# Performance work log

Hardware: AMD Instinct MI355X
Metric: run time of the kernel (lower is better)

## Reference

```python
import jax, jax.numpy as jnp
import numpy as np

NUM_GRAPHS = 128
EPS = 1e-5  # torch BatchNorm1d default eps


def setup_inputs() -> dict:
    key = jax.random.key(0)
    ks = jax.random.split(key, 24)
    N, E, NHE = 50000, 800000, 50000
    NODE_RAW, HEDGE_RAW, H, HH, HOUT = 92, 40, 128, 128, 256
    s = 0.05
    inp = {
        "x": jax.random.normal(ks[0], (N, NODE_RAW), jnp.float32),
        "hedge_attrs": jax.random.normal(ks[1], (NHE, HEDGE_RAW), jnp.float32),
        "inter_relations_index": jax.random.randint(ks[2], (3, E), 0, N, jnp.int64),
        "batch": jax.random.randint(ks[3], (N,), 0, NUM_GRAPHS, jnp.int64),
        "num_nodes": N,
        # embed: Linear(92, h_dim)
        "embed_w": jax.random.normal(ks[4], (NODE_RAW, H), jnp.float32) * s,
        "embed_b": jax.random.normal(ks[5], (H,), jnp.float32) * s,
        # bembed: Linear(hedge_dim, hidden_hedge_dim)
        "bembed_w": jax.random.normal(ks[6], (HEDGE_RAW, HH), jnp.float32) * s,
        "bembed_b": jax.random.normal(ks[7], (HH,), jnp.float32) * s,
        # conv.lin_full_presplit: Linear(2H+HH, 2H)
        "lin_w": jax.random.normal(ks[8], (2 * H + HH, 2 * H), jnp.float32) * s,
        "lin_b": jax.random.normal(ks[9], (2 * H,), jnp.float32) * s,
        "bn1_g": jnp.ones((2 * H,), jnp.float32),
        "bn1_b": jnp.zeros((2 * H,), jnp.float32),
        "bn2_g": jnp.ones((H,), jnp.float32),
        "bn2_b": jnp.zeros((H,), jnp.float32),
        # learnable temperature of SoftmaxAggregation (init 1.0)
        "aggr_t": jnp.ones((), jnp.float32),
        "l1_w": jax.random.normal(ks[10], (H, HOUT), jnp.float32) * s,
        "l1_b": jax.random.normal(ks[11], (HOUT,), jnp.float32) * s,
        "out_w": jax.random.normal(ks[12], (HOUT, 1), jnp.float32) * s,
        "out_b": jax.random.normal(ks[13], (1,), jnp.float32) * s,
    }
    return inp


def _batchnorm(z, g, b):
    mu = z.mean(axis=0)
    var = z.var(axis=0)  # biased, matching torch training-mode normalization
    return (z - mu) * jax.lax.rsqrt(var + EPS) * g + b


def reference(x, hedge_attrs, inter_relations_index, batch, num_nodes,
              embed_w, embed_b, bembed_w, bembed_b, lin_w, lin_b,
              bn1_g, bn1_b, bn2_g, bn2_b, aggr_t, l1_w, l1_b, out_w, out_b):
    idx0 = inter_relations_index[0]
    idx1 = inter_relations_index[1]
    connect_feats = hedge_attrs @ bembed_w + bembed_b          # [NHE, HH]
    h = x @ embed_w + embed_b                                   # [N, H]

    # --- CHGInterConv ---
    origin = h[idx0]                                            # [E, H]
    connect = connect_feats[idx1]                               # [E, HH]
    remote = h[idx0]                                            # faithful to source (uses idx0)
    z = jnp.concatenate([origin, connect, remote], axis=1)      # [E, 2H+HH]
    z = z @ lin_w + lin_b                                       # [E, 2H]
    z = _batchnorm(z, bn1_g, bn1_b)
    z_f, z_c = jnp.split(z, 2, axis=-1)
    msg = jax.nn.sigmoid(z_f) * jax.nn.softplus(z_c)            # [E, H]

    # learned SoftmaxAggregation: per-node, per-channel segment softmax of t*msg
    alpha = msg * aggr_t
    m = jax.ops.segment_max(alpha, idx0, num_segments=num_nodes)
    m = jnp.where(jnp.isfinite(m), m, 0.0)                      # empty segments
    e = jnp.exp(alpha - m[idx0])
    denom = jax.ops.segment_sum(e, idx0, num_segments=num_nodes)
    w = e / (denom[idx0] + 1e-16)
    out = jax.ops.segment_sum(msg * w, idx0, num_segments=num_nodes)  # [N, H]

    out = _batchnorm(out, bn2_g, bn2_b)
    h = jax.nn.softplus(out + h)                                # residual + softplus

    # --- global mean pool over graphs ---
    counts = jax.ops.segment_sum(jnp.ones((num_nodes,), h.dtype), batch,
                                 num_segments=NUM_GRAPHS)
    pooled = jax.ops.segment_sum(h, batch, num_segments=NUM_GRAPHS)
    pooled = pooled / jnp.maximum(counts, 1.0)[:, None]         # [G, H]

    g = jax.nn.softplus(pooled @ l1_w + l1_b)                   # [G, HOUT]
    return g @ out_w + out_b                                    # [G, 1]
```

## Files before the change

kernel.cpp:

```cpp
#include <hip/hip_runtime.h>
#include <hip/hip_bf16.h>


#define EPS_BN 1e-5f
#define LOG2E 1.4426950408889634f
#define LN2   0.6931471805599453f

#define BIN_SH 8
#define BIN_CHUNK 4096

typedef __attribute__((ext_vector_type(8))) short bf16x8;
typedef __attribute__((ext_vector_type(4))) float f32x4;
typedef __attribute__((ext_vector_type(2))) float f32x2;

__device__ __forceinline__ float fexp2(float x) {
#if __has_builtin(__builtin_amdgcn_exp2f)
    return __builtin_amdgcn_exp2f(x);
#else
    return __expf(x * LN2);
#endif
}
__device__ __forceinline__ float flog2(float x) {
#if __has_builtin(__builtin_amdgcn_logf)
    return __builtin_amdgcn_logf(x);
#else
    return __logf(x) * LOG2E;
#endif
}
__device__ __forceinline__ float softplus_fast(float x) {
    return LN2 * flog2(1.f + fexp2(x * LOG2E));
}

__device__ __forceinline__ f32x2 pk_fma2(f32x2 a, f32x2 b, f32x2 c) {
#if __has_builtin(__builtin_elementwise_fma)
    return __builtin_elementwise_fma(a, b, c);
#else
    return (f32x2){fmaf(a.x, b.x, c.x), fmaf(a.y, b.y, c.y)};
#endif
}

__device__ __forceinline__ unsigned short f2bf(float f) {
    unsigned u = __float_as_uint(f);
    unsigned r = (u + 0x7fffu + ((u >> 16) & 1u)) >> 16;
    return (unsigned short)r;
}
__device__ __forceinline__ float bflo(unsigned u) { return __uint_as_float(u << 16); }
__device__ __forceinline__ float bfhi(unsigned u) { return __uint_as_float(u & 0xffff0000u); }
__device__ __forceinline__ float bfu16(unsigned short v) { return __uint_as_float(((unsigned)v) << 16); }
__device__ __forceinline__ unsigned pack2bf(float x, float y) {
    return (unsigned)f2bf(x) | ((unsigned)f2bf(y) << 16);
}

#if __has_builtin(__builtin_amdgcn_cvt_pk_f32_fp8) && __has_builtin(__builtin_amdgcn_cvt_pk_fp8_f32)
#define HW_FP8 1
#else
#define HW_FP8 0
#endif

__device__ __forceinline__ unsigned char f2fp8(float f) {
#if HW_FP8
    int r = __builtin_amdgcn_cvt_pk_fp8_f32(f, f, 0, false);
    return (unsigned char)(r & 0xff);
#else
    unsigned u = __float_as_uint(f);
    unsigned s = (u >> 24) & 0x80u;
    float af = fabsf(f);
    if (!(af >= 0.015625f)) {
        int m = (int)rintf(af * 512.f);
        if (m > 7) m = 7;
        return (unsigned char)(s | (unsigned)m);
    }
    if (af > 448.f) return (unsigned char)(s | 0x7e);
    unsigned au = __float_as_uint(af);
    unsigned r = au + 0x7ffffu + ((au >> 20) & 1u);
    int e8 = (int)(r >> 23) - 120;
    unsigned m = (r >> 20) & 7u;
    if (e8 > 15 || (e8 == 15 && m == 7)) return (unsigned char)(s | 0x7e);
    return (unsigned char)(s | ((unsigned)e8 << 3) | m);
#endif
}

__device__ __forceinline__ void fp8pair(unsigned p, f32x2& lo, f32x2& hi) {
#if HW_FP8
    lo = __builtin_amdgcn_cvt_pk_f32_fp8((int)p, false);
    hi = __builtin_amdgcn_cvt_pk_f32_fp8((int)p, true);
#else
    auto dec = [](unsigned byte) -> float {
        unsigned s = (byte & 0x80u) << 24;
        unsigned em = byte & 0x7fu;
        float nrm = __uint_as_float(s | ((em << 20) + 0x3C000000u));
        float sub = __uint_as_float(s | 0x3F800000u) * (float)em * 0.001953125f;
        return (em >= 8) ? nrm : sub;
    };
    lo = (f32x2){dec(p & 0xff), dec((p >> 8) & 0xff)};
    hi = (f32x2){dec((p >> 16) & 0xff), dec(p >> 24)};
#endif
}

__device__ __forceinline__ int perm256(int j) {
    return (j < 128) ? ((j >> 1) * 4 + (j & 1)) : (((j - 128) >> 1) * 4 + 2 + (j & 1));
}

__global__ __launch_bounds__(256) void k_pre(const float* __restrict__ ew, const float* __restrict__ bw,
                                             const float* __restrict__ lw,
                                             unsigned short* __restrict__ embB, unsigned short* __restrict__ bembB,
                                             unsigned short* __restrict__ waB, unsigned short* __restrict__ wcB,
                                             const int* __restrict__ idx0, const int* __restrict__ batch,
                                             int* __restrict__ bsum, int* __restrict__ gcount,
                                             int E, int N, int NB) {
    const int t = threadIdx.x;
    const int bid = blockIdx.x;
    if (bid >= 320) {
        __shared__ int lhist[256];
        __shared__ int lbat[128];
        const int cb = bid - 320;
        lhist[t] = 0;
        if (t < 128) lbat[t] = 0;
        __syncthreads();
        const int e0 = cb * BIN_CHUNK;
        const int ecnt = min(E - e0, BIN_CHUNK);
        for (int i = t; i < ecnt; i += 256)
            atomicAdd(&lhist[idx0[e0 + i] >> BIN_SH], 1);
        const int n0 = cb * BIN_CHUNK;
        const int ncnt = min(N - n0, BIN_CHUNK);
        for (int i = t; i < ncnt; i += 256)
            atomicAdd(&lbat[batch[n0 + i]], 1);
        __syncthreads();
        if (t < NB && lhist[t]) atomicAdd(&bsum[t], lhist[t]);
        if (t < 128 && lbat[t]) atomicAdd(&gcount[t], lbat[t]);
        return;
    }
    int i = bid * 256 + t;
    if (i >= 81920) return;
    unsigned short* dst;
    int f, NKC, CT, mode;
    if (i < 12288)      { dst = embB;  f = i;         NKC = 3; CT = 2; mode = 0; }
    else if (i < 20480) { dst = bembB; f = i - 12288; NKC = 2; CT = 2; mode = 1; }
    else if (i < 53248) { dst = waB;   f = i - 20480; NKC = 4; CT = 4; mode = 2; }
    else                { dst = wcB;   f = i - 53248; NKC = 4; CT = 4; mode = 3; }
    int j = f & 7, l = (f >> 3) & 63;
    int r2 = f >> 9;
    int c = r2 % CT;
    int r3 = r2 / CT;
    int kc = r3 % NKC, w = r3 / NKC;
    int k = kc * 32 + ((l >> 4) & 3) * 8 + j;
    int n = (w * CT + c) * 16 + (l & 15);
    float v;
    if (mode == 0)      v = (k < 92) ? ew[k * 128 + n] : 0.f;
    else if (mode == 1) v = (k < 40) ? bw[k * 128 + n] : 0.f;
    else if (mode == 2) v = lw[k * 256 + n] + lw[(k + 256) * 256 + n];
    else                v = lw[(k + 128) * 256 + n];
    dst[f] = f2bf(v);
}

__global__ __launch_bounds__(256) void k_scanB(const int* __restrict__ bsum, int* __restrict__ boff,
                                               const int* __restrict__ gcount, int* __restrict__ gptr, int NB) {
    __shared__ int s[256];
    const int t = threadIdx.x;
    int v = (t < NB) ? bsum[t] : 0;
    s[t] = v;
    __syncthreads();
#pragma unroll
    for (int ofs = 1; ofs < 256; ofs <<= 1) {
        int u = (t >= ofs) ? s[t - ofs] : 0;
        __syncthreads();
        s[t] += u;
        __syncthreads();
    }
    if (t < NB) boff[t] = s[t] - v;
    if (t == NB - 1) boff[NB] = s[t];
    __syncthreads();
    int gv = (t < 128) ? gcount[t] : 0;
    s[t] = gv;
    __syncthreads();
#pragma unroll
    for (int ofs = 1; ofs < 128; ofs <<= 1) {
        int u = (t >= ofs && t < 128) ? s[t - ofs] : 0;
        __syncthreads();
        if (t < 128) s[t] += u;
        __syncthreads();
    }
    if (t < 128) gptr[t + 1] = s[t];
    if (t == 0) gptr[0] = 0;
}

__global__ __launch_bounds__(256) void k_scatterpos(const int* __restrict__ batch, const int* __restrict__ gptr,
                                                    int* __restrict__ gfill, int* __restrict__ pos_of, int N) {
    int i = blockIdx.x * 256 + threadIdx.x;
    if (i < N) {
        int g = batch[i];
        pos_of[i] = gptr[g] + atomicAdd(&gfill[g], 1);
    }
}

template<int KIN, int NKC1, int OMODE2>
__global__ __launch_bounds__(256) void mfma_fused(
    const float* __restrict__ in, const unsigned short* __restrict__ B1, const float* __restrict__ bias1,
    const unsigned short* __restrict__ B2, const float* __restrict__ bias2,
    unsigned short* __restrict__ hout, void* __restrict__ out2, int M,
    const int* __restrict__ pos_of)
{
    const int r0 = blockIdx.x * 32;
    const int t = threadIdx.x;
    const int w = t >> 6;
    const int l = t & 63;
    const int m = l & 15, q = l >> 4;

    __shared__ __align__(16) unsigned short als[32 * NKC1 * 32];
    __shared__ __align__(16) unsigned short hls[32 * 136];

    const int KP = NKC1 * 32;
    for (int i = t; i < 32 * KP; i += 256) {
        int r = i / KP, k = i - r * KP;
        int gr = r0 + r;
        float v = (gr < M && k < KIN) ? in[(size_t)gr * KIN + k] : 0.f;
        int idx = (((r >> 4) * NKC1 + (k >> 5)) * 64 + ((k >> 3) & 3) * 16 + (r & 15)) * 8 + (k & 7);
        als[idx] = f2bf(v);
    }
    bf16x8 b1[NKC1][2];
    const bf16x8* B1f = (const bf16x8*)B1;
#pragma unroll
    for (int kc = 0; kc < NKC1; kc++)
#pragma unroll
        for (int c = 0; c < 2; c++)
            b1[kc][c] = B1f[((w * NKC1 + kc) * 2 + c) * 64 + l];
    __syncthreads();

    f32x4 acc1[2][2];
#pragma unroll
    for (int c = 0; c < 2; c++) { acc1[c][0] = (f32x4){0.f,0.f,0.f,0.f}; acc1[c][1] = (f32x4){0.f,0.f,0.f,0.f}; }
    const bf16x8* af = (const bf16x8*)als;
#pragma unroll
    for (int kc = 0; kc < NKC1; kc++) {
        bf16x8 a0 = af[kc * 64 + l];
        bf16x8 a1 = af[(NKC1 + kc) * 64 + l];
#pragma unroll
        for (int c = 0; c < 2; c++) {
            acc1[c][0] = __builtin_amdgcn_mfma_f32_16x16x32_bf16(a0, b1[kc][c], acc1[c][0], 0, 0, 0);
            acc1[c][1] = __builtin_amdgcn_mfma_f32_16x16x32_bf16(a1, b1[kc][c], acc1[c][1], 0, 0, 0);
        }
    }
#pragma unroll
    for (int c = 0; c < 2; c++) {
        int n1 = (w * 2 + c) * 16 + m;
        float bv = bias1[n1];
#pragma unroll
        for (int hh = 0; hh < 2; hh++) {
#pragma unroll
            for (int r = 0; r < 4; r++) {
                int row = hh * 16 + q * 4 + r;
                float val = acc1[c][hh][r] + bv;
                unsigned short bf = f2bf(val);
                hls[row * 136 + n1] = bf;
                if (OMODE2 == 1 && r0 + row < M)
                    hout[(size_t)pos_of[r0 + row] * 128 + n1] = bf;
            }
        }
    }
    __syncthreads();

    bf16x8 b2[4][4];
    const bf16x8* B2f = (const bf16x8*)B2;
#pragma unroll
    for (int kc = 0; kc < 4; kc++)
#pragma unroll
        for (int c = 0; c < 4; c++)
            b2[kc][c] = B2f[((w * 4 + kc) * 4 + c) * 64 + l];

    f32x4 acc2[4][2];
#pragma unroll
    for (int c = 0; c < 4; c++) { acc2[c][0] = (f32x4){0.f,0.f,0.f,0.f}; acc2[c][1] = (f32x4){0.f,0.f,0.f,0.f}; }
#pragma unroll
    for (int kc = 0; kc < 4; kc++) {
        bf16x8 a0 = *(const bf16x8*)(hls + m * 136 + kc * 32 + q * 8);
        bf16x8 a1 = *(const bf16x8*)(hls + (m + 16) * 136 + kc * 32 + q * 8);
#pragma unroll
        for (int c = 0; c < 4; c++) {
            acc2[c][0] = __builtin_amdgcn_mfma_f32_16x16x32_bf16(a0, b2[kc][c], acc2[c][0], 0, 0, 0);
            acc2[c][1] = __builtin_amdgcn_mfma_f32_16x16x32_bf16(a1, b2[kc][c], acc2[c][1], 0, 0, 0);
        }
    }
#pragma unroll
    for (int c = 0; c < 4; c++) {
        int n = (w * 4 + c) * 16 + m;
        float bv = bias2 ? bias2[n] : 0.f;
        int pj = perm256(n);
#pragma unroll
        for (int hh = 0; hh < 2; hh++) {
#pragma unroll
            for (int r = 0; r < 4; r++) {
                int row = r0 + hh * 16 + q * 4 + r;
                if (row < M) {
                    float val = acc2[c][hh][r] + bv;
                    if (OMODE2 == 1) ((unsigned short*)out2)[(size_t)row * 256 + pj] = f2bf(val);
                    else             ((unsigned char*)out2)[(size_t)row * 256 + pj] = f2fp8(val);
                }
            }
        }
    }
}

__global__ __launch_bounds__(256) void k_binA(
    const int* __restrict__ idx0, const int* __restrict__ idx1,
    const int* __restrict__ boff, int* __restrict__ bfill,
    int* __restrict__ staging, int E, int NB)
{
    const int t = threadIdx.x;
    const int bid = blockIdx.x;
    __shared__ int svals[BIN_CHUNK];
    __shared__ unsigned char sbk[BIN_CHUNK];
    __shared__ int lhist[256], lbase[256];
    const int e0 = bid * BIN_CHUNK;
    const int cnt = min(E - e0, BIN_CHUNK);
    for (int b = t; b < NB; b += 256) lhist[b] = 0;
    __syncthreads();
    for (int i = t; i < cnt; i += 256) {
        int n = idx0[e0 + i];
        int m = idx1[e0 + i];
        int bk = n >> BIN_SH;
        sbk[i] = (unsigned char)bk;
        svals[i] = (m << BIN_SH) | (n & ((1 << BIN_SH) - 1));
        atomicAdd(&lhist[bk], 1);
    }
    __syncthreads();
    for (int b = t; b < NB; b += 256) {
        int h = lhist[b];
        int base = h ? atomicAdd(&bfill[b], h) : 0;
        lbase[b] = boff[b] + base;
        lhist[b] = 0;
    }
    __syncthreads();
    for (int i = t; i < cnt; i += 256) {
        int bk = sbk[i];
        int r = atomicAdd(&lhist[bk], 1);
        staging[lbase[bk] + r] = svals[i];
    }
}

__global__ __launch_bounds__(256) void k_binB(
    const int* __restrict__ boff, const int* __restrict__ staging,
    int* __restrict__ rowptr, int* __restrict__ sidx1, int* __restrict__ slots,
    int E, int N, int per_slot)
{
    __shared__ int lcnt[256];
    __shared__ int noofs[256];
    __shared__ int s[256];
    const int t = threadIdx.x;
    const int b = blockIdx.x;
    const int n0 = b << BIN_SH;
    const int nn = min(N - n0, 256);
    const int s0 = boff[b], s1 = boff[b + 1];
    lcnt[t] = 0;
    __syncthreads();
    for (int i = s0 + t; i < s1; i += 256)
        atomicAdd(&lcnt[staging[i] & 255], 1);
    __syncthreads();
    int v = lcnt[t];
    s[t] = v;
    __syncthreads();
#pragma unroll
    for (int ofs = 1; ofs < 256; ofs <<= 1) {
        int u = (t >= ofs) ? s[t - ofs] : 0;
        __syncthreads();
        s[t] += u;
        __syncthreads();
    }
    noofs[t] = s[t] - v;
    if (t < nn) rowptr[n0 + t] = s0 + s[t] - v;
    lcnt[t] = 0;
    if (b == 0 && t == 0) rowptr[N] = E;
    __syncthreads();
    if (s1 > s0) {
        int sfirst = (s0 + per_slot - 1) / per_slot;
        int slast  = (s1 - 1) / per_slot;
        for (int si = sfirst + t; si <= slast; si += 256) {
            int tgt = si * per_slot - s0;
            int lo = 0, hi = nn;
            while (lo + 1 < hi) {
                int mid = (lo + hi) >> 1;
                if (noofs[mid] <= tgt) lo = mid; else hi = mid;
            }
            slots[si] = n0 + lo;
        }
    }
    for (int i = s0 + t; i < s1; i += 256) {
        int vv = staging[i];
        int nl = vv & 255;
        int r = atomicAdd(&lcnt[nl], 1);
        sidx1[s0 + noofs[nl] + r] = vv & 0xffffff00;
    }
}

__global__ __launch_bounds__(256) void k_stats(const uint2* __restrict__ A16, const unsigned char* __restrict__ Cp8b,
                                               const int* __restrict__ rowptr, const int* __restrict__ sidx1,
                                               const int* __restrict__ slots,
                                               float* __restrict__ gsum, float* __restrict__ gsq,
                                               int E, int N, int per_slot) {
    __shared__ float4 lsm4[256], lsq4[256];
    const int t = threadIdx.x;
    const int l = t & 63;
    const int wid = __builtin_amdgcn_readfirstlane(t >> 6);
    const int slot = blockIdx.x * 4 + wid;
    const unsigned lo4 = (unsigned)(l << 2);
    const long base = (long)slot * per_slot;
    const int e0 = (int)min((long)E, base);
    const int e1 = (int)min((long)E, base + per_slot);
    f32x2 smF = {0.f,0.f}, smC = {0.f,0.f};
    f32x2 sqF = {0.f,0.f}, sqC = {0.f,0.f};
    f32x2 csrF = {0.f,0.f}, csrC = {0.f,0.f};
    f32x2 aF = {0.f,0.f}, aC = {0.f,0.f};
    int cur_n = 0, bound = 0, runk = 0;

    auto flush = [&]() {
        if (runk) {
            float fk = (float)runk;
            f32x2 fk2 = {fk, fk};
            smF += csrF; smC += csrC;
            smF = pk_fma2(fk2, aF, smF);
            smC = pk_fma2(fk2, aC, smC);
            f32x2 tF = pk_fma2(fk2, aF, csrF + csrF);
            f32x2 tC = pk_fma2(fk2, aC, csrC + csrC);
            sqF = pk_fma2(aF, tF, sqF);
            sqC = pk_fma2(aC, tC, sqC);
        }
        csrF = (f32x2){0.f,0.f}; csrC = (f32x2){0.f,0.f};
        runk = 0;
    };
    auto loadA = [&](int n) {
        uint2 a8 = A16[(size_t)n * 64 + l];
        aF = (f32x2){bflo(a8.x), bfhi(a8.x)};
        aC = (f32x2){bflo(a8.y), bfhi(a8.y)};
    };

    if (e0 < e1) {
        cur_n = __builtin_amdgcn_readfirstlane(slots[slot]);
        bound = __builtin_amdgcn_readfirstlane(rowptr[cur_n + 1]);
        loadA(cur_n);
    }

    auto proc = [&](int e, unsigned p) {
        if (e >= bound) {
            flush();
            do { cur_n++; bound = __builtin_amdgcn_readfirstlane(rowptr[cur_n + 1]); } while (bound <= e);
            loadA(cur_n);
        }
        f32x2 vf, vc;
        fp8pair(p, vf, vc);
        csrF += vf; csrC += vc;
        sqF = pk_fma2(vf, vf, sqF);
        sqC = pk_fma2(vc, vc, sqC);
        runk++;
    };

    const int nfull = (e1 - e0) & ~7;
    if (nfull > 0) {
        int eg = e0;
        unsigned cur[8];
        {
            int4 m0 = *(const int4*)(sidx1 + eg);
            int4 m1 = *(const int4*)(sidx1 + eg + 4);
            cur[0] = *(const unsigned*)(Cp8b + ((unsigned)m0.x + lo4));
            cur[1] = *(const unsigned*)(Cp8b + ((unsigned)m0.y + lo4));
            cur[2] = *(const unsigned*)(Cp8b + ((unsigned)m0.z + lo4));
            cur[3] = *(const unsigned*)(Cp8b + ((unsigned)m0.w + lo4));
            cur[4] = *(const unsigned*)(Cp8b + ((unsigned)m1.x + lo4));
            cur[5] = *(const unsigned*)(Cp8b + ((unsigned)m1.y + lo4));
            cur[6] = *(const unsigned*)(Cp8b + ((unsigned)m1.z + lo4));
            cur[7] = *(const unsigned*)(Cp8b + ((unsigned)m1.w + lo4));
        }
        for (;;) {
            const int en = eg + 8;
            const bool more = en < e0 + nfull;
            unsigned nxt[8];
            if (more) {
                int4 t0 = *(const int4*)(sidx1 + en);
                int4 t1 = *(const int4*)(sidx1 + en + 4);
                nxt[0] = *(const unsigned*)(Cp8b + ((unsigned)t0.x + lo4));
                nxt[1] = *(const unsigned*)(Cp8b + ((unsigned)t0.y + lo4));
                nxt[2] = *(const unsigned*)(Cp8b + ((unsigned)t0.z + lo4));
                nxt[3] = *(const unsigned*)(Cp8b + ((unsigned)t0.w + lo4));
                nxt[4] = *(const unsigned*)(Cp8b + ((unsigned)t1.x + lo4));
                nxt[5] = *(const unsigned*)(Cp8b + ((unsigned)t1.y + lo4));
                nxt[6] = *(const unsigned*)(Cp8b + ((unsigned)t1.z + lo4));
                nxt[7] = *(const unsigned*)(Cp8b + ((unsigned)t1.w + lo4));
            }
            proc(eg, cur[0]);     proc(eg + 1, cur[1]);
            proc(eg + 2, cur[2]); proc(eg + 3, cur[3]);
            proc(eg + 4, cur[4]); proc(eg + 5, cur[5]);
            proc(eg + 6, cur[6]); proc(eg + 7, cur[7]);
            if (!more) break;
#pragma unroll
            for (int i = 0; i < 8; i++) cur[i] = nxt[i];
            eg = en;
        }
    }
    for (int e = e0 + nfull; e < e1; e++)
        proc(e, *(const unsigned*)(Cp8b + ((unsigned)sidx1[e] + lo4)));
    flush();

    lsm4[t] = (float4){smF.x, smF.y, smC.x, smC.y};
    lsq4[t] = (float4){sqF.x, sqF.y, sqC.x, sqC.y};
    __syncthreads();
    const float* fm = (const float*)lsm4;
    const float* fq = (const float*)lsq4;
    float vs = fm[t] + fm[256 + t] + fm[512 + t] + fm[768 + t];
    float vq = fq[t] + fq[256 + t] + fq[512 + t] + fq[768 + t];
    atomicAdd(&gsum[t], vs);
    atomicAdd(&gsq[t], vq);
}

__global__ __launch_bounds__(256) void k_aggr(const uint2* __restrict__ A16, const unsigned char* __restrict__ Cp8b,
                                              const int* __restrict__ rowptr, const int* __restrict__ sidx1,
                                              const int* __restrict__ pos_of,
                                              const float* __restrict__ bn1_sum, const float* __restrict__ bn1_sq,
                                              const float* __restrict__ g1, const float* __restrict__ b1,
                                              const float* __restrict__ tptr, unsigned* __restrict__ out,
                                              float invE, int N) {
    const int t = threadIdx.x;
    const int l = t & 63;
    const int wid = __builtin_amdgcn_readfirstlane(t >> 6);
    const int n = blockIdx.x * 4 + wid;
    if (n >= N) return;

    const int e0 = __builtin_amdgcn_readfirstlane(rowptr[n]);
    const int e1 = __builtin_amdgcn_readfirstlane(rowptr[n + 1]);
    const int pn = __builtin_amdgcn_readfirstlane(pos_of[n]);

    const float tt = tptr[0];
    const float4 sum4 = ((const float4*)bn1_sum)[l];
    const float4 sq4  = ((const float4*)bn1_sq)[l];
    const float2 gf = ((const float2*)g1)[l];
    const float2 gc = ((const float2*)(g1 + 128))[l];
    const float2 bf2 = ((const float2*)b1)[l];
    const float2 bc2 = ((const float2*)(b1 + 128))[l];
    auto mkss = [&](float sum, float sq, float gg, float bb, float& sc, float& sh) {
        float mu = sum * invE;
        float var = sq * invE - mu * mu;
        sc = gg * rsqrtf(var + EPS_BN);
        sh = fmaf(-mu, sc, bb);
    };
    float scx, shx, scy, shy, scz, shz, scw, shw;
    mkss(sum4.x, sq4.x, gf.x, bf2.x, scx, shx);
    mkss(sum4.y, sq4.y, gf.y, bf2.y, scy, shy);
    mkss(sum4.z, sq4.z, gc.x, bc2.x, scz, shz);
    mkss(sum4.w, sq4.w, gc.y, bc2.y, scw, shw);
    const f32x2 sF  = {-scx * LOG2E, -scy * LOG2E};
    const f32x2 sC  = { scz * LOG2E,  scw * LOG2E};

    uint2 a8 = A16[(size_t)n * 64 + l];
    f32x2 aF = {bflo(a8.x), bfhi(a8.x)}, aC = {bflo(a8.y), bfhi(a8.y)};
    const f32x2 bF = pk_fma2(aF, sF, (f32x2){-shx * LOG2E, -shy * LOG2E});
    const f32x2 bC = pk_fma2(aC, sC, (f32x2){ shz * LOG2E,  shw * LOG2E});

    if (e0 >= e1) { out[(size_t)pn * 64 + l] = 0u; return; }

    const unsigned lo4 = (unsigned)(l << 2);
    f32x2 den = {0.f,0.f}, num = {0.f,0.f};

    auto G = [&](int e) -> unsigned {
        return *(const unsigned*)(Cp8b + ((unsigned)sidx1[e] + lo4));
    };
    auto procg = [&](unsigned p) {
        f32x2 vf, vc;
        fp8pair(p, vf, vc);
        f32x2 argf = pk_fma2(vf, sF, bF);
        f32x2 argc = pk_fma2(vc, sC, bC);
        f32x2 ef = {fexp2(argf.x), fexp2(argf.y)};
        f32x2 uu = {fexp2(argc.x), fexp2(argc.y)};
        f32x2 d1 = ef + 1.f;
        f32x2 u1 = uu + 1.f;
        f32x2 sig = {__builtin_amdgcn_rcpf(d1.x), __builtin_amdgcn_rcpf(d1.y)};
        f32x2 lg = {flog2(u1.x), flog2(u1.y)};
        f32x2 M = sig * lg;
        f32x2 tM = M * tt;
        f32x2 w = {fexp2(tM.x), fexp2(tM.y)};
        den += w;
        num = pk_fma2(M, w, num);
    };

    const int cnt = e1 - e0;
    unsigned cur[8];
#pragma unroll
    for (int i = 0; i < 8; i++)
        if (i < cnt) cur[i] = G(e0 + i);

    int e = e0;
    while (e + 8 < e1) {
        unsigned nxt[8];
#pragma unroll
        for (int i = 0; i < 8; i++)
            if (e + 8 + i < e1) nxt[i] = G(e + 8 + i);
#pragma unroll
        for (int i = 0; i < 8; i++) procg(cur[i]);
#pragma unroll
        for (int i = 0; i < 8; i++) cur[i] = nxt[i];
        e += 8;
    }
    const int rem = e1 - e;
#pragma unroll
    for (int i = 0; i < 8; i++)
        if (i < rem) procg(cur[i]);

    float ox = LN2 * num.x * __builtin_amdgcn_rcpf(den.x);
    float oy = LN2 * num.y * __builtin_amdgcn_rcpf(den.y);
    out[(size_t)pn * 64 + l] = pack2bf(ox, oy);
}

__global__ __launch_bounds__(256) void k_bn2stats(const unsigned* __restrict__ outw, float* __restrict__ sum,
                                                  float* __restrict__ sq, int N) {
    __shared__ float4 ls[256];
    const int t = threadIdx.x;
    const int w = t & 63;
    const int rg = t >> 6;
    f32x2 sm = {0.f,0.f}, s2 = {0.f,0.f};
    for (int n = blockIdx.x * 4 + rg; n < N; n += gridDim.x * 4) {
        unsigned v = outw[(size_t)n * 64 + w];
        f32x2 x = {bflo(v), bfhi(v)};
        sm += x;
        s2 = pk_fma2(x, x, s2);
    }
    ls[t] = (float4){sm.x, sm.y, s2.x, s2.y};
    __syncthreads();
    if (t < 64) {
        float4 a = ls[t], b = ls[t + 64], c = ls[t + 128], d = ls[t + 192];
        atomicAdd(&sum[2 * w],     a.x + b.x + c.x + d.x);
        atomicAdd(&sum[2 * w + 1], a.y + b.y + c.y + d.y);
        atomicAdd(&sq[2 * w],      a.z + b.z + c.z + d.z);
        atomicAdd(&sq[2 * w + 1],  a.w + b.w + c.w + d.w);
    }
}

template<int SPLIT>
__global__ __launch_bounds__(128) void k_h2pool(const unsigned short* __restrict__ out,
                                                const unsigned short* __restrict__ h,
                                                const int* __restrict__ gptr,
                                                const float* __restrict__ bn2_sum, const float* __restrict__ bn2_sq,
                                                const float* __restrict__ g2, const float* __restrict__ b2,
                                                float* __restrict__ pooled, float invN) {
    const int g = blockIdx.x & 127;
    const int sp = blockIdx.x >> 7;
    const int c = threadIdx.x;
    float mu = bn2_sum[c] * invN;
    float var = bn2_sq[c] * invN - mu * mu;
    float sc = g2[c] * rsqrtf(var + EPS_BN);
    float sh = fmaf(-mu, sc, b2[c]);
    const int i0 = gptr[g], i1 = gptr[g + 1];
    float acc = 0.f;
    for (int i = i0 + sp; i < i1; i += SPLIT) {
        float v = fmaf(bfu16(out[(size_t)i * 128 + c]), sc, sh) + bfu16(h[(size_t)i * 128 + c]);
        acc += softplus_fast(v);
    }
    if (acc != 0.f) atomicAdd(&pooled[g * 128 + c], acc);
}

__global__ __launch_bounds__(256) void k_head(const float* __restrict__ pooled, const int* __restrict__ gcount,
                                              const float* __restrict__ l1w, const float* __restrict__ l1b,
                                              const float* __restrict__ outw, const float* __restrict__ outb,
                                              float* __restrict__ dout) {
    __shared__ float p[128];
    __shared__ float red[256];
    const int g = blockIdx.x;
    const int j = threadIdx.x;
    if (j < 128) {
        float cnt = (float)max(gcount[g], 1);
        p[j] = pooled[g * 128 + j] / cnt;
    }
    __syncthreads();
    float acc = l1b[j];
    for (int k = 0; k < 128; k++) acc = fmaf(p[k], l1w[k * 256 + j], acc);
    red[j] = softplus_fast(acc) * outw[j];
    __syncthreads();
    for (int s = 128; s > 0; s >>= 1) {
        if (j < s) red[j] += red[j + s];
        __syncthreads();
    }
    if (j == 0) dout[g] = red[0] + outb[0];
}

extern "C" void kernel_launch(void* const* d_in, const int* in_sizes, int n_in,
                              void* d_out, int out_size, void* d_ws, size_t ws_size,
                              hipStream_t stream) {
    const float* x        = (const float*)d_in[0];
    const float* hedge    = (const float*)d_in[1];
    const int*   iri      = (const int*)d_in[2];
    const int*   batch    = (const int*)d_in[3];
    const float* embed_w  = (const float*)d_in[5];
    const float* embed_b  = (const float*)d_in[6];
    const float* bembed_w = (const float*)d_in[7];
    const float* bembed_b = (const float*)d_in[8];
    const float* lin_w    = (const float*)d_in[9];
    const float* lin_b    = (const float*)d_in[10];
    const float* bn1_g    = (const float*)d_in[11];
    const float* bn1_b    = (const float*)d_in[12];
    const float* bn2_g    = (const float*)d_in[13];
    const float* bn2_b    = (const float*)d_in[14];
    const float* aggr_t   = (const float*)d_in[15];
    const float* l1_w     = (const float*)d_in[16];
    const float* l1_b     = (const float*)d_in[17];
    const float* out_w    = (const float*)d_in[18];
    const float* out_b    = (const float*)d_in[19];

    const int N   = in_sizes[0] / 92;
    const int NHE = in_sizes[1] / 40;
    const int E   = in_sizes[2] / 3;
    const int* idx0 = iri;
    const int* idx1 = iri + E;

    float* ws = (float*)d_ws;
    size_t off = 0;
    auto alloc = [&](size_t elems) -> float* {
        float* p = ws + off;
        off += (elems + 63) & ~(size_t)63;
        return p;
    };
    unsigned short* h16 = (unsigned short*)alloc((size_t)N * 64);
    uint2* A16    = (uint2*)alloc((size_t)N * 128);
    unsigned* Cp8 = (unsigned*)alloc((size_t)NHE * 64);
    unsigned short* embB  = (unsigned short*)alloc(6144);
    unsigned short* bembB = (unsigned short*)alloc(4096);
    unsigned short* waB   = (unsigned short*)alloc(16384);
    unsigned short* wcB   = (unsigned short*)alloc(16384);
    int*   rowptr = (int*)alloc((size_t)N + 1);
    int*   boff   = (int*)alloc(260);
    int*   sidx1  = (int*)alloc((size_t)E + 8);
    int*   staging = (int*)alloc((size_t)E + 8);
    int*   gptr   = (int*)alloc(129);
    int*   pos_of = (int*)alloc((size_t)N);
    int*   slots  = (int*)alloc(8200);
    unsigned* outbuf = (unsigned*)alloc((size_t)N * 64);
    float* zbase  = ws + off;
    int*   bsum   = (int*)alloc(256);
    int*   bfill  = (int*)alloc(256);
    int*   gfill  = (int*)alloc(128);
    int*   gcount = (int*)alloc(128);
    float* bn1_sum = alloc(256);
    float* bn1_sq  = alloc(256);
    float* bn2_sum = alloc(128);
    float* bn2_sq  = alloc(128);
    float* pooled  = alloc(128 * 128);
    size_t zbytes = (size_t)((ws + off) - zbase) * sizeof(float);
    (void)ws_size;

    hipMemsetAsync(zbase, 0, zbytes, stream);

    const int NB = (N + 255) >> BIN_SH;
    const int EB = (E + BIN_CHUNK - 1) / BIN_CHUNK;

    k_pre<<<320 + EB, 256, 0, stream>>>(embed_w, bembed_w, lin_w, embB, bembB, waB, wcB,
                                        idx0, batch, bsum, gcount, E, N, NB);
    k_scanB<<<1, 256, 0, stream>>>(bsum, boff, gcount, gptr, NB);
    k_scatterpos<<<(N + 255) / 256, 256, 0, stream>>>(batch, gptr, gfill, pos_of, N);

    const int mtN   = (N + 31) / 32;
    const int mtNHE = (NHE + 31) / 32;
    mfma_fused<92, 3, 1><<<mtN, 256, 0, stream>>>(x, embB, embed_b, waB, lin_b, h16, A16, N, pos_of);
    mfma_fused<40, 2, 2><<<mtNHE, 256, 0, stream>>>(hedge, bembB, bembed_b, wcB, nullptr, nullptr, Cp8, NHE,
                                                    nullptr);

    const int EDGE_BLOCKS = 2048;
    const int NSLOTS = EDGE_BLOCKS * 4;
    int per_slot = ((E + NSLOTS - 1) / NSLOTS + 7) & ~7;
    k_binA<<<EB, 256, 0, stream>>>(idx0, idx1, boff, bfill, staging, E, NB);
    k_binB<<<NB, 256, 0, stream>>>(boff, staging, rowptr, sidx1, slots, E, N, per_slot);

    k_stats<<<EDGE_BLOCKS, 256, 0, stream>>>(A16, (const unsigned char*)Cp8, rowptr, sidx1, slots,
                                             bn1_sum, bn1_sq, E, N, per_slot);

    k_aggr<<<(N + 3) / 4, 256, 0, stream>>>(A16, (const unsigned char*)Cp8, rowptr, sidx1, pos_of,
                                            bn1_sum, bn1_sq, bn1_g, bn1_b, aggr_t, outbuf,
                                            1.0f / (float)E, N);

    k_bn2stats<<<256, 256, 0, stream>>>((const unsigned*)outbuf, bn2_sum, bn2_sq, N);
    k_h2pool<16><<<128 * 16, 128, 0, stream>>>((const unsigned short*)outbuf, h16, gptr,
                                               bn2_sum, bn2_sq, bn2_g, bn2_b, pooled, 1.0f / (float)N);

    k_head<<<128, 256, 0, stream>>>(pooled, gcount, l1_w, l1_b, out_w, out_b, (float*)d_out);
}
```

Baseline: 411.4 us.

## Merge scan with scatterpos and fuse both GEMMs with edge binning into one launch

Folds the scatter-position pass into the scan kernel: every block recomputes the 128-graph prefix locally, so the separate launch and the dependency on gptr go away. The two MFMA GEMM kernels and the k_binA edge-binning kernel are merged into one k_main launch that dispatches by block index and uses a shared char buffer for scratch. This cuts kernel launches and lets the independent GEMM and binning work run concurrently on the GPU. In exchange, shared memory per block is sized for the largest branch, which may reduce occupancy for the GEMM blocks.

After: 386.0 us (median of 2 runs). -6.2%, faster.

```diff
diff --git a/kernel.cpp b/kernel.cpp
--- a/kernel.cpp
+++ b/kernel.cpp
@@ -153,23 +153,42 @@
     dst[f] = f2bf(v);
 }
 
-__global__ __launch_bounds__(256) void k_scanB(const int* __restrict__ bsum, int* __restrict__ boff,
-                                               const int* __restrict__ gcount, int* __restrict__ gptr, int NB) {
+__global__ __launch_bounds__(256) void k_scan(const int* __restrict__ bsum, int* __restrict__ boff,
+                                              const int* __restrict__ gcount, int* __restrict__ gptr,
+                                              const int* __restrict__ batch, int* __restrict__ gfill,
+                                              int* __restrict__ pos_of, int N, int NB) {
     __shared__ int s[256];
     const int t = threadIdx.x;
-    int v = (t < NB) ? bsum[t] : 0;
-    s[t] = v;
-    __syncthreads();
-#pragma unroll
-    for (int ofs = 1; ofs < 256; ofs <<= 1) {
-        int u = (t >= ofs) ? s[t - ofs] : 0;
-        __syncthreads();
-        s[t] += u;
-        __syncthreads();
-    }
-    if (t < NB) boff[t] = s[t] - v;
-    if (t == NB - 1) boff[NB] = s[t];
-    __syncthreads();
+    const int bid = blockIdx.x;
+    if (bid == 0) {
+        int v = (t < NB) ? bsum[t] : 0;
+        s[t] = v;
+        __syncthreads();
+#pragma unroll
+        for (int ofs = 1; ofs < 256; ofs <<= 1) {
+            int u = (t >= ofs) ? s[t - ofs] : 0;
+            __syncthreads();
+            s[t] += u;
+            __syncthreads();
+        }
+        if (t < NB) boff[t] = s[t] - v;
+        if (t == NB - 1) boff[NB] = s[t];
+        __syncthreads();
+        int gv = (t < 128) ? gcount[t] : 0;
+        s[t] = gv;
+        __syncthreads();
+#pragma unroll
+        for (int ofs = 1; ofs < 128; ofs <<= 1) {
+            int u = (t >= ofs && t < 128) ? s[t - ofs] : 0;
+            __syncthreads();
+            if (t < 128) s[t] += u;
+            __syncthreads();
+        }
+        if (t < 128) gptr[t + 1] = s[t];
+        if (t == 0) gptr[0] = 0;
+        return;
+    }
+    __shared__ int lg[128];
     int gv = (t < 128) ? gcount[t] : 0;
     s[t] = gv;
     __syncthreads();
@@ -180,34 +199,31 @@
         if (t < 128) s[t] += u;
         __syncthreads();
     }
-    if (t < 128) gptr[t + 1] = s[t];
-    if (t == 0) gptr[0] = 0;
-}
-
-__global__ __launch_bounds__(256) void k_scatterpos(const int* __restrict__ batch, const int* __restrict__ gptr,
-                                                    int* __restrict__ gfill, int* __restrict__ pos_of, int N) {
-    int i = blockIdx.x * 256 + threadIdx.x;
+    if (t < 128) lg[t] = s[t] - gv;
+    __syncthreads();
+    int i = (bid - 1) * 256 + t;
     if (i < N) {
         int g = batch[i];
-        pos_of[i] = gptr[g] + atomicAdd(&gfill[g], 1);
+        pos_of[i] = lg[g] + atomicAdd(&gfill[g], 1);
     }
 }
 
 template<int KIN, int NKC1, int OMODE2>
-__global__ __launch_bounds__(256) void mfma_fused(
+__device__ __forceinline__ void gemm_body(
+    char* smem, int blk,
     const float* __restrict__ in, const unsigned short* __restrict__ B1, const float* __restrict__ bias1,
     const unsigned short* __restrict__ B2, const float* __restrict__ bias2,
     unsigned short* __restrict__ hout, void* __restrict__ out2, int M,
     const int* __restrict__ pos_of)
 {
-    const int r0 = blockIdx.x * 32;
+    const int r0 = blk * 32;
     const int t = threadIdx.x;
     const int w = t >> 6;
     const int l = t & 63;
     const int m = l & 15, q = l >> 4;
 
-    __shared__ __align__(16) unsigned short als[32 * NKC1 * 32];
-    __shared__ __align__(16) unsigned short hls[32 * 136];
+    unsigned short* als = (unsigned short*)smem;
+    unsigned short* hls = als + 32 * NKC1 * 32;
 
     const int KP = NKC1 * 32;
     for (int i = t; i < 32 * KP; i += 256) {
@@ -300,17 +316,18 @@
     }
 }
 
-__global__ __launch_bounds__(256) void k_binA(
+__device__ __forceinline__ void binA_body(
+    char* smem, int cb,
     const int* __restrict__ idx0, const int* __restrict__ idx1,
     const int* __restrict__ boff, int* __restrict__ bfill,
     int* __restrict__ staging, int E, int NB)
 {
     const int t = threadIdx.x;
-    const int bid = blockIdx.x;
-    __shared__ int svals[BIN_CHUNK];
-    __shared__ unsigned char sbk[BIN_CHUNK];
-    __shared__ int lhist[256], lbase[256];
-    const int e0 = bid * BIN_CHUNK;
+    int* svals = (int*)smem;
+    unsigned char* sbk = (unsigned char*)(smem + 16384);
+    int* lhist = (int*)(smem + 20480);
+    int* lbase = (int*)(smem + 21504);
+    const int e0 = cb * BIN_CHUNK;
     const int cnt = min(E - e0, BIN_CHUNK);
     for (int b = t; b < NB; b += 256) lhist[b] = 0;
     __syncthreads();
@@ -334,6 +351,27 @@
         int bk = sbk[i];
         int r = atomicAdd(&lhist[bk], 1);
         staging[lbase[bk] + r] = svals[i];
+    }
+}
+
+__global__ __launch_bounds__(256) void k_main(
+    const float* __restrict__ x, const unsigned short* __restrict__ embB, const float* __restrict__ embed_b,
+    const unsigned short* __restrict__ waB, const float* __restrict__ lin_b,
+    unsigned short* __restrict__ h16, uint2* __restrict__ A16, int N, const int* __restrict__ pos_of,
+    const float* __restrict__ hedge, const unsigned short* __restrict__ bembB, const float* __restrict__ bembed_b,
+    const unsigned short* __restrict__ wcB, unsigned* __restrict__ Cp8, int NHE,
+    const int* __restrict__ idx0, const int* __restrict__ idx1,
+    const int* __restrict__ boff, int* __restrict__ bfill, int* __restrict__ staging,
+    int E, int NB, int mtN, int mtNHE)
+{
+    __shared__ __align__(16) char smem[22528];
+    const int bid = blockIdx.x;
+    if (bid < mtN) {
+        gemm_body<92, 3, 1>(smem, bid, x, embB, embed_b, waB, lin_b, h16, (void*)A16, N, pos_of);
+    } else if (bid < mtN + mtNHE) {
+        gemm_body<40, 2, 2>(smem, bid - mtN, hedge, bembB, bembed_b, wcB, nullptr, nullptr, (void*)Cp8, NHE, nullptr);
+    } else {
+        binA_body(smem, bid - mtN - mtNHE, idx0, idx1, boff, bfill, staging, E, NB);
     }
 }
 
@@ -745,22 +783,23 @@
 
     const int NB = (N + 255) >> BIN_SH;
     const int EB = (E + BIN_CHUNK - 1) / BIN_CHUNK;
+    const int GB = (N + 255) / 256;
 
     k_pre<<<320 + EB, 256, 0, stream>>>(embed_w, bembed_w, lin_w, embB, bembB, waB, wcB,
                                         idx0, batch, bsum, gcount, E, N, NB);
-    k_scanB<<<1, 256, 0, stream>>>(bsum, boff, gcount, gptr, NB);
-    k_scatterpos<<<(N + 255) / 256, 256, 0, stream>>>(batch, gptr, gfill, pos_of, N);
+
+    k_scan<<<1 + GB, 256, 0, stream>>>(bsum, boff, gcount, gptr, batch, gfill, pos_of, N, NB);
 
     const int mtN   = (N + 31) / 32;
     const int mtNHE = (NHE + 31) / 32;
-    mfma_fused<92, 3, 1><<<mtN, 256, 0, stream>>>(x, embB, embed_b, waB, lin_b, h16, A16, N, pos_of);
-    mfma_fused<40, 2, 2><<<mtNHE, 256, 0, stream>>>(hedge, bembB, bembed_b, wcB, nullptr, nullptr, Cp8, NHE,
-                                                    nullptr);
+    k_main<<<mtN + mtNHE + EB, 256, 0, stream>>>(
+        x, embB, embed_b, waB, lin_b, h16, A16, N, pos_of,
+        hedge, bembB, bembed_b, wcB, Cp8, NHE,
+        idx0, idx1, boff, bfill, staging, E, NB, mtN, mtNHE);
 
     const int EDGE_BLOCKS = 2048;
     const int NSLOTS = EDGE_BLOCKS * 4;
     int per_slot = ((E + NSLOTS - 1) / NSLOTS + 7) & ~7;
-    k_binA<<<EB, 256, 0, stream>>>(idx0, idx1, boff, bfill, staging, E, NB);
     k_binB<<<NB, 256, 0, stream>>>(boff, staging, rowptr, sidx1, slots, E, N, per_slot);
 
     k_stats<<<EDGE_BLOCKS, 256, 0, stream>>>(A16, (const unsigned char*)Cp8, rowptr, sidx1, slots,
```
